# Performance work log

Hardware: AMD Instinct MI355X
Metric: run time of the kernel (lower is better)

## Reference

```python
import jax, jax.numpy as jnp
import numpy as np
import math

N = 100000
E = 800000
H = 256
TDIM = 32
NTYPES = 22
NLAYERS = 2


def layer_norm(x, g, b, eps=1e-5):
    mu = jnp.mean(x, axis=-1, keepdims=True)
    var = jnp.var(x, axis=-1, keepdims=True)
    return (x - mu) * jax.lax.rsqrt(var + eps) * g + b


def setup_inputs() -> dict:
    key = jax.random.key(0)
    ks = jax.random.split(key, 16)
    s = 1.0 / math.sqrt(H)
    inp = {
        "clause_reprs": jax.random.normal(ks[0], (N, H), dtype=jnp.float32),
        "timestamps": jax.random.uniform(ks[1], (N,), dtype=jnp.float32) * 10000.0,
        "deriv_types": jax.random.randint(ks[2], (N,), 0, NTYPES),
        "derivation_edges": jax.random.randint(ks[3], (2, E), 0, N),
        # params
        "emb_table": jax.random.normal(ks[4], (NTYPES, H), dtype=jnp.float32),
        "temp_W": jax.random.normal(ks[5], (TDIM, H), dtype=jnp.float32) / math.sqrt(TDIM),
        "temp_b": jnp.zeros((H,), jnp.float32),
        "fus_W1": jax.random.normal(ks[6], (3 * H, H), dtype=jnp.float32) / math.sqrt(3 * H),
        "fus_b1": jnp.zeros((H,), jnp.float32),
        "fus_W2": jax.random.normal(ks[7], (H, H), dtype=jnp.float32) * s,
        "fus_b2": jnp.zeros((H,), jnp.float32),
        "in_g": jnp.ones((H,), jnp.float32),
        "in_b": jnp.zeros((H,), jnp.float32),
        "deriv_W": jax.random.normal(ks[8], (NLAYERS, 2 * H, H), dtype=jnp.float32) / math.sqrt(2 * H),
        "deriv_b": jnp.zeros((NLAYERS, H), jnp.float32),
        "dn_g": jnp.ones((NLAYERS, H), jnp.float32),
        "dn_b": jnp.zeros((NLAYERS, H), jnp.float32),
    }
    return inp


def reference(clause_reprs, timestamps, deriv_types, derivation_edges,
              emb_table, temp_W, temp_b, fus_W1, fus_b1, fus_W2, fus_b2,
              in_g, in_b, deriv_W, deriv_b, dn_g, dn_b):
    # --- temporal sinusoidal encoding -> projection ---
    half = TDIM // 2
    freqs = jnp.exp(-math.log(10000.0) * jnp.arange(half, dtype=jnp.float32) / half)
    angles = timestamps[:, None] * freqs[None, :]                      # (N, half)
    pe = jnp.concatenate([jnp.sin(angles), jnp.cos(angles)], axis=-1)  # (N, TDIM)
    temporal_enc = pe @ temp_W + temp_b                                # (N, H)
    # --- derivation type embedding ---
    deriv_enc = emb_table[deriv_types]                                 # (N, H)
    # --- input fusion + residual + LN ---
    cat = jnp.concatenate([clause_reprs, temporal_enc, deriv_enc], axis=-1)
    fused = jax.nn.relu(cat @ fus_W1 + fus_b1) @ fus_W2 + fus_b2
    x = layer_norm(fused + clause_reprs, in_g, in_b)
    # --- derivation message passing along DAG edges (parent -> child) ---
    src, dst = derivation_edges[0], derivation_edges[1]
    count = jnp.zeros((N, 1), jnp.float32).at[dst].add(1.0)
    count = jnp.maximum(count, 1.0)
    for l in range(NLAYERS):
        parent_msgs = x[src]                                           # (E, H) gather
        agg = jnp.zeros_like(x).at[dst].add(parent_msgs) / count       # (N, H) scatter-add
        combined = jnp.concatenate([x, agg], axis=-1)                  # (N, 2H)
        update = jax.nn.relu(combined @ deriv_W[l] + deriv_b[l])
        x = layer_norm(x + update, dn_g[l], dn_b[l])
    return x
```

## Files before the change

### kernel.cpp

```cpp
#include <hip/hip_runtime.h>
#include <hip/hip_bf16.h>
#include <math.h>

#define N_NODES 100000
#define N_EDGES 800000
#define H 256
#define NTYPES 22
#define SCAN_G 98
#define GRID5 ((N_NODES + 127) / 128)

typedef __attribute__((ext_vector_type(8))) short short8;
typedef __attribute__((ext_vector_type(4))) float f32x4;
typedef unsigned short u16;

__device__ __forceinline__ u16 f2bf(float f) {
    unsigned u = __float_as_uint(f);
    u += 0x7FFF + ((u >> 16) & 1);
    return (u16)(u >> 16);
}
__device__ __forceinline__ float bf2f(u16 u) {
    return __uint_as_float(((unsigned)u) << 16);
}
__device__ __forceinline__ int pi2(int k) {
    return (k & 192) | ((k & 3) << 4) | ((k >> 2) & 15);
}

__device__ __forceinline__ void gload16(const void* g, void* l) {
    __builtin_amdgcn_global_load_lds(
        (const __attribute__((address_space(1))) unsigned int*)g,
        (__attribute__((address_space(3))) unsigned int*)l, 16, 0, 0);
}

__global__ __launch_bounds__(256) void conv_bf16(
    const float* __restrict__ src, u16* __restrict__ dst)
{
    size_t i = (size_t)blockIdx.x * 256 + threadIdx.x;
    const float4 a = ((const float4*)src)[i * 2];
    const float4 b = ((const float4*)src)[i * 2 + 1];
    short8 v;
    v[0] = (short)f2bf(a.x); v[1] = (short)f2bf(a.y);
    v[2] = (short)f2bf(a.z); v[3] = (short)f2bf(a.w);
    v[4] = (short)f2bf(b.x); v[5] = (short)f2bf(b.y);
    v[6] = (short)f2bf(b.z); v[7] = (short)f2bf(b.w);
    ((short8*)dst)[i] = v;
}

__global__ __launch_bounds__(256) void prep_small(
    const float* __restrict__ temp_W, const float* __restrict__ temp_b,
    const float* __restrict__ emb, const float* __restrict__ fus_W1,
    const float* __restrict__ fus_b1,
    float* __restrict__ C1, float* __restrict__ C2, float* __restrict__ beff)
{
    int b = blockIdx.x;
    int j = threadIdx.x;
    if (b < 32) {
        float acc = 0.f;
        #pragma unroll 8
        for (int m = 0; m < H; ++m)
            acc += temp_W[b * H + m] * fus_W1[(size_t)(H + m) * H + j];
        C1[b * H + j] = acc;
    } else if (b < 32 + NTYPES) {
        int e = b - 32;
        float acc = 0.f;
        #pragma unroll 8
        for (int m = 0; m < H; ++m)
            acc += emb[e * H + m] * fus_W1[(size_t)(2 * H + m) * H + j];
        C2[e * H + j] = acc;
    } else {
        float acc = fus_b1[j];
        #pragma unroll 8
        for (int m = 0; m < H; ++m)
            acc += temp_b[m] * fus_W1[(size_t)(H + m) * H + j];
        beff[j] = acc;
    }
}

__global__ __launch_bounds__(256) void prep_frag(
    const float* __restrict__ fus_W1, const float* __restrict__ C1,
    const float* __restrict__ fus_W2, const float* __restrict__ deriv_W,
    u16* __restrict__ wblob)
{
    int s = blockIdx.x;
    #pragma unroll
    for (int it = 0; it < 4; ++it) {
        int c = it * 256 + threadIdx.x;
        int l = c & 63, nt = c >> 6;
        int ncol = (nt << 4) | (l & 15);
        int kin = (l >> 4) << 3;
        short8 v;
        #pragma unroll
        for (int i = 0; i < 8; ++i) {
            const float* srcp;
            if (s < 8) {
                srcp = fus_W1 + (size_t)(s * 32 + kin + i) * H;
            } else if (s == 8) {
                srcp = C1 + (size_t)(kin + i) * H;
            } else if (s < 17) {
                int k = (s - 9) * 32 + kin + i;
                srcp = fus_W2 + (size_t)pi2(k) * H;
            } else if (s < 33) {
                int k = (s - 17) * 32 + kin + i;
                srcp = deriv_W + (size_t)((k >> 8) * 256 + pi2(k & 255)) * H;
            } else {
                int k = (s - 33) * 32 + kin + i;
                srcp = deriv_W + (size_t)(512 + (k >> 8) * 256 + pi2(k & 255)) * H;
            }
            v[i] = (short)f2bf(srcp[ncol]);
        }
        *reinterpret_cast<short8*>(wblob + (size_t)s * 8192 + (size_t)c * 8) = v;
    }
}

__global__ void count_kernel(const int* __restrict__ dst, int* __restrict__ cnt)
{
    int e = blockIdx.x * blockDim.x + threadIdx.x;
    if (e < N_EDGES) atomicAdd(&cnt[dst[e]], 1);
}

__global__ __launch_bounds__(1024) void scan1_kernel(
    const int* __restrict__ cnt, int* __restrict__ off, int* __restrict__ bsum)
{
    __shared__ int s[1024];
    int i = blockIdx.x * 1024 + threadIdx.x;
    int v = (i < N_NODES) ? cnt[i] : 0;
    s[threadIdx.x] = v;
    __syncthreads();
    #pragma unroll
    for (int o = 1; o < 1024; o <<= 1) {
        int t = (threadIdx.x >= o) ? s[threadIdx.x - o] : 0;
        __syncthreads();
        s[threadIdx.x] += t;
        __syncthreads();
    }
    if (i < N_NODES) off[i] = s[threadIdx.x];
    if (threadIdx.x == 1023) bsum[blockIdx.x] = s[1023];
}

__global__ void scan2_kernel(const int* __restrict__ bsum, int* __restrict__ bbase)
{
    if (threadIdx.x == 0) {
        int acc = 0;
        for (int b = 0; b < SCAN_G; ++b) { bbase[b] = acc; acc += bsum[b]; }
    }
}

__global__ __launch_bounds__(1024) void scan3_kernel(
    int* __restrict__ off, const int* __restrict__ bbase,
    const int* __restrict__ cnt, int* __restrict__ cursor)
{
    int i = blockIdx.x * 1024 + threadIdx.x;
    if (i < N_NODES) {
        int incl = off[i] + bbase[blockIdx.x];
        off[i] = incl;
        cursor[i] = incl - cnt[i];
    }
}

__global__ void fill_kernel(const int* __restrict__ src, const int* __restrict__ dst,
                            int* __restrict__ cursor, int* __restrict__ csr)
{
    int e = blockIdx.x * blockDim.x + threadIdx.x;
    if (e < N_EDGES) {
        int pos = atomicAdd(&cursor[dst[e]], 1);
        csr[pos] = src[e];
    }
}

__global__ __launch_bounds__(256) void gather_kernel(
    const u16* __restrict__ xb, const int* __restrict__ csr,
    const int* __restrict__ off, const int* __restrict__ cnt,
    u16* __restrict__ agg)
{
    int node = blockIdx.x * 4 + (threadIdx.x >> 6);
    int l = threadIdx.x & 63;
    int deg = cnt[node];
    int start = off[node] - deg;
    float a0 = 0.f, a1 = 0.f, a2 = 0.f, a3 = 0.f;
    float b0 = 0.f, b1 = 0.f, b2 = 0.f, b3 = 0.f;
    int j = 0;
    for (; j + 1 < deg; j += 2) {
        int s0 = csr[start + j], s1 = csr[start + j + 1];
        ushort4 v0 = *reinterpret_cast<const ushort4*>(xb + (size_t)s0 * H + l * 4);
        ushort4 v1 = *reinterpret_cast<const ushort4*>(xb + (size_t)s1 * H + l * 4);
        a0 += bf2f(v0.x); a1 += bf2f(v0.y); a2 += bf2f(v0.z); a3 += bf2f(v0.w);
        b0 += bf2f(v1.x); b1 += bf2f(v1.y); b2 += bf2f(v1.z); b3 += bf2f(v1.w);
    }
    if (j < deg) {
        int s0 = csr[start + j];
        ushort4 v0 = *reinterpret_cast<const ushort4*>(xb + (size_t)s0 * H + l * 4);
        a0 += bf2f(v0.x); a1 += bf2f(v0.y); a2 += bf2f(v0.z); a3 += bf2f(v0.w);
    }
    float sc = 1.0f / fmaxf((float)deg, 1.0f);
    ushort4 o;
    o.x = f2bf((a0 + b0) * sc); o.y = f2bf((a1 + b1) * sc);
    o.z = f2bf((a2 + b2) * sc); o.w = f2bf((a3 + b3) * sc);
    *reinterpret_cast<ushort4*>(agg + (size_t)node * H + l * 4) = o;
}

__device__ __forceinline__ void stageA8(u16* Af, const u16* __restrict__ src,
                                        int i0, int kbase, int tid)
{
    int rt = tid >> 6, l = tid & 63;
    int row = min(i0 + rt * 16 + (l & 15), N_NODES - 1);
    gload16(src + (size_t)row * H + kbase + ((l >> 4) << 3), Af + (tid << 3));
}

__device__ __forceinline__ void stageB8(u16* Bf, const u16* __restrict__ wk, int tid)
{
    gload16(wk + ((size_t)tid << 3),         Bf + (tid << 3));
    gload16(wk + ((size_t)(tid + 512) << 3), Bf + ((tid + 512) << 3));
}

__device__ __forceinline__ void mfma_step8(const u16* Af, const u16* Bf,
                                           int wm, int wn, int l, f32x4 acc[4][4])
{
    short8 a[4], b[4];
    #pragma unroll
    for (int m = 0; m < 4; ++m)
        a[m] = *reinterpret_cast<const short8*>(Af + ((((wm << 2) | m) << 6 | l) << 3));
    #pragma unroll
    for (int n = 0; n < 4; ++n)
        b[n] = *reinterpret_cast<const short8*>(Bf + ((((wn << 2) | n) << 6 | l) << 3));
    #pragma unroll
    for (int n = 0; n < 4; ++n)
        #pragma unroll
        for (int m = 0; m < 4; ++m)
            acc[m][n] = __builtin_amdgcn_mfma_f32_16x16x32_bf16(a[m], b[n],
                                                                acc[m][n], 0, 0, 0);
}

__global__ __launch_bounds__(512, 4) void k1_mfma(
    const u16* __restrict__ cb, const float* __restrict__ ts,
    const int* __restrict__ types, const u16* __restrict__ wblob,
    const float* __restrict__ C2, const float* __restrict__ beff,
    u16* __restrict__ hb)
{
    __shared__ __align__(16) u16 Af[4096];
    __shared__ __align__(16) u16 Bf[8192];
    int tid = threadIdx.x, w = tid >> 6, l = tid & 63;
    int wm = w >> 2, wn = w & 3, g = l >> 4, c0 = l & 15;
    int i0 = blockIdx.x * 128;
    f32x4 acc[4][4] = {};

    for (int t = 0; t < 9; ++t) {
        if (t < 8) {
            stageA8(Af, cb, i0, t * 32, tid);
        } else {
            int rt = tid >> 6;
            int row = min(i0 + rt * 16 + c0, N_NODES - 1);
            float tsv = ts[row];
            short8 v;
            #pragma unroll
            for (int i = 0; i < 8; ++i) {
                int k = (g << 3) + i;
                float fr = expf(-0.57564627324851f * (float)(k & 15));
                float ang = tsv * fr;
                float pv = (k < 16) ? sinf(ang) : cosf(ang);
                v[i] = (short)f2bf(pv);
            }
            *reinterpret_cast<short8*>(Af + (tid << 3)) = v;
        }
        stageB8(Bf, wblob + (size_t)t * 8192, tid);
        __syncthreads();
        mfma_step8(Af, Bf, wm, wn, l, acc);
        __syncthreads();
    }

    float bev[4];
    #pragma unroll
    for (int n = 0; n < 4; ++n) bev[n] = beff[(((wn << 2) | n) << 4) | c0];
    #pragma unroll
    for (int m = 0; m < 4; ++m) {
        #pragma unroll
        for (int r = 0; r < 4; ++r) {
            int rl = (((wm << 2) | m) << 4) + (g << 2) + r;
            int row = i0 + rl;
            bool ok = row < N_NODES;
            int tp = types[ok ? row : 0];
            const float* c2r = C2 + (size_t)tp * H;
            ushort4 o;
            float v0 = fmaxf(acc[m][0][r] + bev[0] + c2r[((wn << 2) << 4) | c0], 0.f);
            float v1 = fmaxf(acc[m][1][r] + bev[1] + c2r[(((wn << 2) | 1) << 4) | c0], 0.f);
            float v2 = fmaxf(acc[m][2][r] + bev[2] + c2r[(((wn << 2) | 2) << 4) | c0], 0.f);
            float v3 = fmaxf(acc[m][3][r] + bev[3] + c2r[(((wn << 2) | 3) << 4) | c0], 0.f);
            o.x = f2bf(v0); o.y = f2bf(v1); o.z = f2bf(v2); o.w = f2bf(v3);
            if (ok)
                *reinterpret_cast<ushort4*>(hb + (size_t)row * H + (wn << 6) + (c0 << 2)) = o;
        }
    }
}

__global__ __launch_bounds__(512, 4) void k2_mfma(
    const u16* __restrict__ hb, const u16* __restrict__ cb,
    const u16* __restrict__ wblob, const float* __restrict__ b2,
    const float* __restrict__ gW, const float* __restrict__ bW,
    u16* __restrict__ xb)
{
    __shared__ __align__(16) u16 Af[4096];
    __shared__ __align__(16) u16 Bf[8192];
    int tid = threadIdx.x, w = tid >> 6, l = tid & 63;
    int wm = w >> 2, wn = w & 3, g = l >> 4, c0 = l & 15;
    int i0 = blockIdx.x * 128;
    f32x4 acc[4][4] = {};

    for (int t = 0; t < 8; ++t) {
        stageA8(Af, hb, i0, t * 32, tid);
        stageB8(Bf, wblob + (size_t)t * 8192, tid);
        __syncthreads();
        mfma_step8(Af, Bf, wm, wn, l, acc);
        __syncthreads();
    }

    float bv[4], gv[4], bbv[4];
    int lc[4];
    #pragma unroll
    for (int n = 0; n < 4; ++n) {
        lc[n] = (((wn << 2) | n) << 4) | c0;
        bv[n] = b2[lc[n]]; gv[n] = gW[lc[n]]; bbv[n] = bW[lc[n]];
    }
    float2* red = reinterpret_cast<float2*>(Af);
    #pragma unroll
    for (int m = 0; m < 4; ++m) {
        #pragma unroll
        for (int r = 0; r < 4; ++r) {
            int rl = (((wm << 2) | m) << 4) + (g << 2) + r;
            int rowc = min(i0 + rl, N_NODES - 1);
            const u16* cr = cb + (size_t)rowc * H;
            float s = 0.f, q = 0.f;
            #pragma unroll
            for (int n = 0; n < 4; ++n) {
                float pv = acc[m][n][r] + bv[n] + bf2f(cr[lc[n]]);
                acc[m][n][r] = pv;
                s += pv; q += pv * pv;
            }
            #pragma unroll
            for (int o = 1; o < 16; o <<= 1) {
                s += __shfl_xor(s, o);
                q += __shfl_xor(q, o);
            }
            if (c0 == 0) red[(rl << 2) | wn] = make_float2(s, q);
        }
    }
    __syncthreads();
    #pragma unroll
    for (int m = 0; m < 4; ++m) {
        #pragma unroll
        for (int r = 0; r < 4; ++r) {
            int rl = (((wm << 2) | m) << 4) + (g << 2) + r;
            int row = i0 + rl;
            float2 t0 = red[(rl << 2) | 0], t1 = red[(rl << 2) | 1];
            float2 t2 = red[(rl << 2) | 2], t3 = red[(rl << 2) | 3];
            float S = t0.x + t1.x + t2.x + t3.x;
            float Q = t0.y + t1.y + t2.y + t3.y;
            float mu = S * (1.0f / 256.0f);
            float rstd = rsqrtf(Q * (1.0f / 256.0f) - mu * mu + 1e-5f);
            if (row < N_NODES) {
                ushort4 o;
                o.x = f2bf((acc[m][0][r] - mu) * rstd * gv[0] + bbv[0]);
                o.y = f2bf((acc[m][1][r] - mu) * rstd * gv[1] + bbv[1]);
                o.z = f2bf((acc[m][2][r] - mu) * rstd * gv[2] + bbv[2]);
                o.w = f2bf((acc[m][3][r] - mu) * rstd * gv[3] + bbv[3]);
                *reinterpret_cast<ushort4*>(xb + (size_t)row * H + (wn << 6) + (c0 << 2)) = o;
            }
        }
    }
}

template<bool FINAL>
__global__ __launch_bounds__(512, 4) void k5_mfma(
    const u16* __restrict__ xb, const u16* __restrict__ aggb,
    const u16* __restrict__ wblob, const float* __restrict__ bl,
    const float* __restrict__ gl, const float* __restrict__ bnl,
    u16* __restrict__ xbout, float* __restrict__ xout)
{
    __shared__ __align__(16) u16 Af[4096];
    __shared__ __align__(16) u16 Bf[8192];
    int tid = threadIdx.x, w = tid >> 6, l = tid & 63;
    int wm = w >> 2, wn = w & 3, g = l >> 4, c0 = l & 15;
    int i0 = blockIdx.x * 128;
    f32x4 acc[4][4] = {};

    for (int t = 0; t < 16; ++t) {
        stageA8(Af, (t < 8) ? xb : aggb, i0, (t & 7) * 32, tid);
        stageB8(Bf, wblob + (size_t)t * 8192, tid);
        __syncthreads();
        mfma_step8(Af, Bf, wm, wn, l, acc);
        __syncthreads();
    }

    float bv[4], gv[4], bbv[4];
    int lc[4];
    #pragma unroll
    for (int n = 0; n < 4; ++n) {
        lc[n] = (((wn << 2) | n) << 4) | c0;
        bv[n] = bl[lc[n]]; gv[n] = gl[lc[n]]; bbv[n] = bnl[lc[n]];
    }
    float2* red = reinterpret_cast<float2*>(Af);
    #pragma unroll
    for (int m = 0; m < 4; ++m) {
        #pragma unroll
        for (int r = 0; r < 4; ++r) {
            int rl = (((wm << 2) | m) << 4) + (g << 2) + r;
            int rowc = min(i0 + rl, N_NODES - 1);
            ushort4 xr = *reinterpret_cast<const ushort4*>(
                xb + (size_t)rowc * H + (wn << 6) + (c0 << 2));
            float s = 0.f, q = 0.f;
            float p0 = bf2f(xr.x) + fmaxf(acc[m][0][r] + bv[0], 0.f);
            float p1 = bf2f(xr.y) + fmaxf(acc[m][1][r] + bv[1], 0.f);
            float p2 = bf2f(xr.z) + fmaxf(acc[m][2][r] + bv[2], 0.f);
            float p3 = bf2f(xr.w) + fmaxf(acc[m][3][r] + bv[3], 0.f);
            acc[m][0][r] = p0; acc[m][1][r] = p1;
            acc[m][2][r] = p2; acc[m][3][r] = p3;
            s = p0 + p1 + p2 + p3;
            q = p0 * p0 + p1 * p1 + p2 * p2 + p3 * p3;
            #pragma unroll
            for (int o = 1; o < 16; o <<= 1) {
                s += __shfl_xor(s, o);
                q += __shfl_xor(q, o);
            }
            if (c0 == 0) red[(rl << 2) | wn] = make_float2(s, q);
        }
    }
    __syncthreads();
    #pragma unroll
    for (int m = 0; m < 4; ++m) {
        #pragma unroll
        for (int r = 0; r < 4; ++r) {
            int rl = (((wm << 2) | m) << 4) + (g << 2) + r;
            int row = i0 + rl;
            float2 t0 = red[(rl << 2) | 0], t1 = red[(rl << 2) | 1];
            float2 t2 = red[(rl << 2) | 2], t3 = red[(rl << 2) | 3];
            float S = t0.x + t1.x + t2.x + t3.x;
            float Q = t0.y + t1.y + t2.y + t3.y;
            float mu = S * (1.0f / 256.0f);
            float rstd = rsqrtf(Q * (1.0f / 256.0f) - mu * mu + 1e-5f);
            if (row < N_NODES) {
                if (FINAL) {
                    #pragma unroll
                    for (int n = 0; n < 4; ++n)
                        xout[(size_t)row * H + lc[n]] =
                            (acc[m][n][r] - mu) * rstd * gv[n] + bbv[n];
                } else {
                    ushort4 o;
                    o.x = f2bf((acc[m][0][r] - mu) * rstd * gv[0] + bbv[0]);
                    o.y = f2bf((acc[m][1][r] - mu) * rstd * gv[1] + bbv[1]);
                    o.z = f2bf((acc[m][2][r] - mu) * rstd * gv[2] + bbv[2]);
                    o.w = f2bf((acc[m][3][r] - mu) * rstd * gv[3] + bbv[3]);
                    *reinterpret_cast<ushort4*>(
                        xbout + (size_t)row * H + (wn << 6) + (c0 << 2)) = o;
                }
            }
        }
    }
}

extern "C" void kernel_launch(void* const* d_in, const int* in_sizes, int n_in,
                              void* d_out, int out_size, void* d_ws, size_t ws_size,
                              hipStream_t stream)
{
    const float* clause  = (const float*)d_in[0];
    const float* ts      = (const float*)d_in[1];
    const int*   types   = (const int*)  d_in[2];
    const int*   edges   = (const int*)  d_in[3];
    const float* emb     = (const float*)d_in[4];
    const float* temp_W  = (const float*)d_in[5];
    const float* temp_b  = (const float*)d_in[6];
    const float* fus_W1  = (const float*)d_in[7];
    const float* fus_b1  = (const float*)d_in[8];
    const float* fus_W2  = (const float*)d_in[9];
    const float* fus_b2  = (const float*)d_in[10];
    const float* in_g    = (const float*)d_in[11];
    const float* in_b    = (const float*)d_in[12];
    const float* deriv_W = (const float*)d_in[13];
    const float* deriv_b = (const float*)d_in[14];
    const float* dn_g    = (const float*)d_in[15];
    const float* dn_b    = (const float*)d_in[16];

    char* p = (char*)d_ws;
    float* C1   = (float*)p;            p += 32 * H * 4;
    float* C2   = (float*)p;            p += NTYPES * H * 4;
    float* beff = (float*)p;            p += H * 4;
    int* cnt    = (int*)p;              p += N_NODES * 4;
    int* off    = (int*)p;              p += N_NODES * 4;
    int* cursor = (int*)p;              p += N_NODES * 4;
    int* bsum   = (int*)p;              p += 128 * 4;
    int* bbase  = (int*)p;              p += 128 * 4;
    int* csr    = (int*)p;              p += N_EDGES * 4;
    u16* wblob  = (u16*)p;              p += 49 * 8192 * 2;
    u16* B1     = (u16*)p;              p += (size_t)N_NODES * H * 2;
    u16* B2     = (u16*)p;              p += (size_t)N_NODES * H * 2;
    float* x    = (float*)d_out;

    const int* src = edges;
    const int* dst = edges + N_EDGES;

    conv_bf16<<<(N_NODES * H / 8 + 255) / 256, 256, 0, stream>>>(clause, B1);
    prep_small<<<32 + NTYPES + 1, 256, 0, stream>>>(temp_W, temp_b, emb, fus_W1,
                                                    fus_b1, C1, C2, beff);
    prep_frag<<<49, 256, 0, stream>>>(fus_W1, C1, fus_W2, deriv_W, wblob);

    hipMemsetAsync(cnt, 0, N_NODES * sizeof(int), stream);
    count_kernel<<<(N_EDGES + 255) / 256, 256, 0, stream>>>(dst, cnt);
    scan1_kernel<<<SCAN_G, 1024, 0, stream>>>(cnt, off, bsum);
    scan2_kernel<<<1, 64, 0, stream>>>(bsum, bbase);
    scan3_kernel<<<SCAN_G, 1024, 0, stream>>>(off, bbase, cnt, cursor);
    fill_kernel<<<(N_EDGES + 255) / 256, 256, 0, stream>>>(src, dst, cursor, csr);

    k1_mfma<<<GRID5, 512, 0, stream>>>(B1, ts, types, wblob, C2, beff, B2);
    k2_mfma<<<GRID5, 512, 0, stream>>>(B2, B1, wblob + (size_t)9 * 8192,
                                       fus_b2, in_g, in_b, B2);

    gather_kernel<<<N_NODES / 4, 256, 0, stream>>>(B2, csr, off, cnt, B1);
    k5_mfma<false><<<GRID5, 512, 0, stream>>>(
        B2, B1, wblob + (size_t)17 * 8192, deriv_b, dn_g, dn_b, B2, nullptr);
    gather_kernel<<<N_NODES / 4, 256, 0, stream>>>(B2, csr, off, cnt, B1);
    k5_mfma<true><<<GRID5, 512, 0, stream>>>(
        B2, B1, wblob + (size_t)33 * 8192, deriv_b + H, dn_g + H, dn_b + H,
        nullptr, x);
}
```

Before: 527.8 us.

## Double-buffer LDS tiles in MFMA GEMMs and widen gather loads to 16 bytes

After: 1.190 ms. +125.6%, slower.

```diff
diff --git a/kernel.cpp b/kernel.cpp
--- a/kernel.cpp
+++ b/kernel.cpp
@@ -173,28 +173,37 @@
 {
     int node = blockIdx.x * 4 + (threadIdx.x >> 6);
     int l = threadIdx.x & 63;
+    int half = l >> 5, lc = l & 31;
     int deg = cnt[node];
     int start = off[node] - deg;
-    float a0 = 0.f, a1 = 0.f, a2 = 0.f, a3 = 0.f;
-    float b0 = 0.f, b1 = 0.f, b2 = 0.f, b3 = 0.f;
-    int j = 0;
-    for (; j + 1 < deg; j += 2) {
-        int s0 = csr[start + j], s1 = csr[start + j + 1];
-        ushort4 v0 = *reinterpret_cast<const ushort4*>(xb + (size_t)s0 * H + l * 4);
-        ushort4 v1 = *reinterpret_cast<const ushort4*>(xb + (size_t)s1 * H + l * 4);
-        a0 += bf2f(v0.x); a1 += bf2f(v0.y); a2 += bf2f(v0.z); a3 += bf2f(v0.w);
-        b0 += bf2f(v1.x); b1 += bf2f(v1.y); b2 += bf2f(v1.z); b3 += bf2f(v1.w);
+    float a[8] = {0.f, 0.f, 0.f, 0.f, 0.f, 0.f, 0.f, 0.f};
+    int j = half;
+    for (; j + 2 < deg; j += 4) {
+        int s0 = csr[start + j];
+        int s1 = csr[start + j + 2];
+        short8 v0 = *reinterpret_cast<const short8*>(xb + (size_t)s0 * H + lc * 8);
+        short8 v1 = *reinterpret_cast<const short8*>(xb + (size_t)s1 * H + lc * 8);
+        #pragma unroll
+        for (int i = 0; i < 8; ++i)
+            a[i] += bf2f((u16)v0[i]) + bf2f((u16)v1[i]);
     }
     if (j < deg) {
         int s0 = csr[start + j];
-        ushort4 v0 = *reinterpret_cast<const ushort4*>(xb + (size_t)s0 * H + l * 4);
-        a0 += bf2f(v0.x); a1 += bf2f(v0.y); a2 += bf2f(v0.z); a3 += bf2f(v0.w);
-    }
-    float sc = 1.0f / fmaxf((float)deg, 1.0f);
-    ushort4 o;
-    o.x = f2bf((a0 + b0) * sc); o.y = f2bf((a1 + b1) * sc);
-    o.z = f2bf((a2 + b2) * sc); o.w = f2bf((a3 + b3) * sc);
-    *reinterpret_cast<ushort4*>(agg + (size_t)node * H + l * 4) = o;
+        short8 v0 = *reinterpret_cast<const short8*>(xb + (size_t)s0 * H + lc * 8);
+        #pragma unroll
+        for (int i = 0; i < 8; ++i)
+            a[i] += bf2f((u16)v0[i]);
+    }
+    #pragma unroll
+    for (int i = 0; i < 8; ++i)
+        a[i] += __shfl_xor(a[i], 32);
+    if (half == 0) {
+        float sc = 1.0f / fmaxf((float)deg, 1.0f);
+        short8 o;
+        #pragma unroll
+        for (int i = 0; i < 8; ++i) o[i] = (short)f2bf(a[i] * sc);
+        *reinterpret_cast<short8*>(agg + (size_t)node * H + lc * 8) = o;
+    }
 }
 
 __device__ __forceinline__ void stageA8(u16* Af, const u16* __restrict__ src,
@@ -229,40 +238,47 @@
                                                                 acc[m][n], 0, 0, 0);
 }
 
-__global__ __launch_bounds__(512, 4) void k1_mfma(
+__global__ __launch_bounds__(512, 6) void k1_mfma(
     const u16* __restrict__ cb, const float* __restrict__ ts,
     const int* __restrict__ types, const u16* __restrict__ wblob,
     const float* __restrict__ C2, const float* __restrict__ beff,
     u16* __restrict__ hb)
 {
-    __shared__ __align__(16) u16 Af[4096];
-    __shared__ __align__(16) u16 Bf[8192];
+    __shared__ __align__(16) u16 Af[2][4096];
+    __shared__ __align__(16) u16 Bf[2][8192];
     int tid = threadIdx.x, w = tid >> 6, l = tid & 63;
     int wm = w >> 2, wn = w & 3, g = l >> 4, c0 = l & 15;
     int i0 = blockIdx.x * 128;
     f32x4 acc[4][4] = {};
 
+    stageA8(Af[0], cb, i0, 0, tid);
+    stageB8(Bf[0], wblob, tid);
+    __syncthreads();
+    #pragma unroll
     for (int t = 0; t < 9; ++t) {
+        int cur = t & 1;
         if (t < 8) {
-            stageA8(Af, cb, i0, t * 32, tid);
-        } else {
-            int rt = tid >> 6;
-            int row = min(i0 + rt * 16 + c0, N_NODES - 1);
-            float tsv = ts[row];
-            short8 v;
-            #pragma unroll
-            for (int i = 0; i < 8; ++i) {
-                int k = (g << 3) + i;
-                float fr = expf(-0.57564627324851f * (float)(k & 15));
-                float ang = tsv * fr;
-                float pv = (k < 16) ? sinf(ang) : cosf(ang);
-                v[i] = (short)f2bf(pv);
-            }
-            *reinterpret_cast<short8*>(Af + (tid << 3)) = v;
-        }
-        stageB8(Bf, wblob + (size_t)t * 8192, tid);
-        __syncthreads();
-        mfma_step8(Af, Bf, wm, wn, l, acc);
+            int t1 = t + 1;
+            if (t1 < 8) {
+                stageA8(Af[cur ^ 1], cb, i0, t1 * 32, tid);
+            } else {
+                int rt = tid >> 6;
+                int row = min(i0 + rt * 16 + c0, N_NODES - 1);
+                float tsv = ts[row];
+                short8 v;
+                #pragma unroll
+                for (int i = 0; i < 8; ++i) {
+                    int k = (g << 3) + i;
+                    float fr = expf(-0.57564627324851f * (float)(k & 15));
+                    float ang = tsv * fr;
+                    float pv = (k < 16) ? sinf(ang) : cosf(ang);
+                    v[i] = (short)f2bf(pv);
+                }
+                *reinterpret_cast<short8*>(Af[cur ^ 1] + (tid << 3)) = v;
+            }
+            stageB8(Bf[cur ^ 1], wblob + (size_t)t1 * 8192, tid);
+        }
+        mfma_step8(Af[cur], Bf[cur], wm, wn, l, acc);
         __syncthreads();
     }
 
@@ -290,24 +306,31 @@
     }
 }
 
-__global__ __launch_bounds__(512, 4) void k2_mfma(
+__global__ __launch_bounds__(512, 6) void k2_mfma(
     const u16* __restrict__ hb, const u16* __restrict__ cb,
     const u16* __restrict__ wblob, const float* __restrict__ b2,
     const float* __restrict__ gW, const float* __restrict__ bW,
     u16* __restrict__ xb)
 {
-    __shared__ __align__(16) u16 Af[4096];
-    __shared__ __align__(16) u16 Bf[8192];
+    __shared__ __align__(16) u16 Af[2][4096];
+    __shared__ __align__(16) u16 Bf[2][8192];
+    __shared__ float2 red[512];
     int tid = threadIdx.x, w = tid >> 6, l = tid & 63;
     int wm = w >> 2, wn = w & 3, g = l >> 4, c0 = l & 15;
     int i0 = blockIdx.x * 128;
     f32x4 acc[4][4] = {};
 
+    stageA8(Af[0], hb, i0, 0, tid);
+    stageB8(Bf[0], wblob, tid);
+    __syncthreads();
+    #pragma unroll
     for (int t = 0; t < 8; ++t) {
-        stageA8(Af, hb, i0, t * 32, tid);
-        stageB8(Bf, wblob + (size_t)t * 8192, tid);
-        __syncthreads();
-        mfma_step8(Af, Bf, wm, wn, l, acc);
+        int cur = t & 1;
+        if (t < 7) {
+            stageA8(Af[cur ^ 1], hb, i0, (t + 1) * 32, tid);
+            stageB8(Bf[cur ^ 1], wblob + (size_t)(t + 1) * 8192, tid);
+        }
+        mfma_step8(Af[cur], Bf[cur], wm, wn, l, acc);
         __syncthreads();
     }
 
@@ -318,7 +341,6 @@
         lc[n] = (((wn << 2) | n) << 4) | c0;
         bv[n] = b2[lc[n]]; gv[n] = gW[lc[n]]; bbv[n] = bW[lc[n]];
     }
-    float2* red = reinterpret_cast<float2*>(Af);
     #pragma unroll
     for (int m = 0; m < 4; ++m) {
         #pragma unroll
@@ -367,24 +389,32 @@
 }
 
 template<bool FINAL>
-__global__ __launch_bounds__(512, 4) void k5_mfma(
+__global__ __launch_bounds__(512, 6) void k5_mfma(
     const u16* __restrict__ xb, const u16* __restrict__ aggb,
     const u16* __restrict__ wblob, const float* __restrict__ bl,
     const float* __restrict__ gl, const float* __restrict__ bnl,
     u16* __restrict__ xbout, float* __restrict__ xout)
 {
-    __shared__ __align__(16) u16 Af[4096];
-    __shared__ __align__(16) u16 Bf[8192];
+    __shared__ __align__(16) u16 Af[2][4096];
+    __shared__ __align__(16) u16 Bf[2][8192];
+    __shared__ float2 red[512];
     int tid = threadIdx.x, w = tid >> 6, l = tid & 63;
     int wm = w >> 2, wn = w & 3, g = l >> 4, c0 = l & 15;
     int i0 = blockIdx.x * 128;
     f32x4 acc[4][4] = {};
 
+    stageA8(Af[0], xb, i0, 0, tid);
+    stageB8(Bf[0], wblob, tid);
+    __syncthreads();
+    #pragma unroll
     for (int t = 0; t < 16; ++t) {
-        stageA8(Af, (t < 8) ? xb : aggb, i0, (t & 7) * 32, tid);
-        stageB8(Bf, wblob + (size_t)t * 8192, tid);
-        __syncthreads();
-        mfma_step8(Af, Bf, wm, wn, l, acc);
+        int cur = t & 1;
+        if (t < 15) {
+            int t1 = t + 1;
+            stageA8(Af[cur ^ 1], (t1 < 8) ? xb : aggb, i0, (t1 & 7) * 32, tid);
+            stageB8(Bf[cur ^ 1], wblob + (size_t)t1 * 8192, tid);
+        }
+        mfma_step8(Af[cur], Bf[cur], wm, wn, l, acc);
         __syncthreads();
     }
 
@@ -395,7 +425,6 @@
         lc[n] = (((wn << 2) | n) << 4) | c0;
         bv[n] = bl[lc[n]]; gv[n] = gl[lc[n]]; bbv[n] = bnl[lc[n]];
     }
-    float2* red = reinterpret_cast<float2*>(Af);
     #pragma unroll
     for (int m = 0; m < 4; ++m) {
         #pragma unroll
@@ -404,15 +433,14 @@
             int rowc = min(i0 + rl, N_NODES - 1);
             ushort4 xr = *reinterpret_cast<const ushort4*>(
                 xb + (size_t)rowc * H + (wn << 6) + (c0 << 2));
-            float s = 0.f, q = 0.f;
             float p0 = bf2f(xr.x) + fmaxf(acc[m][0][r] + bv[0], 0.f);
             float p1 = bf2f(xr.y) + fmaxf(acc[m][1][r] + bv[1], 0.f);
             float p2 = bf2f(xr.z) + fmaxf(acc[m][2][r] + bv[2], 0.f);
             float p3 = bf2f(xr.w) + fmaxf(acc[m][3][r] + bv[3], 0.f);
             acc[m][0][r] = p0; acc[m][1][r] = p1;
             acc[m][2][r] = p2; acc[m][3][r] = p3;
-            s = p0 + p1 + p2 + p3;
-            q = p0 * p0 + p1 * p1 + p2 * p2 + p3 * p3;
+            float s = p0 + p1 + p2 + p3;
+            float q = p0 * p0 + p1 * p1 + p2 * p2 + p3 * p3;
             #pragma unroll
             for (int o = 1; o < 16; o <<= 1) {
                 s += __shfl_xor(s, o);
```
